# Kernel optimization log

Measured on AMD Instinct MI355X. Metric: run time of the kernel, lower is better.

The kernel has to match this reference:

```python
import jax, jax.numpy as jnp
import numpy as np

NE, NPROC, E, D = 50000, 25000, 200000, 128
L, T = 3, 4  # layers, edge types: 0:e->e, 1:e->p, 2:p->p, 3:p->e


def setup_inputs() -> dict:
    key = jax.random.key(0)
    ks = jax.random.split(key, 17)
    s = 1.0 / np.sqrt(D)
    return {
        'x_elem': jax.random.normal(ks[0], (NE, D), jnp.float32),
        'x_proc': jax.random.normal(ks[1], (NPROC, D), jnp.float32),
        'W_src': jax.random.normal(ks[2], (L, T, D, D), jnp.float32) * s,
        'W_dst': jax.random.normal(ks[3], (L, T, D, D), jnp.float32) * s,
        'att_src': jax.random.normal(ks[4], (L, T, D), jnp.float32) * s,
        'att_dst': jax.random.normal(ks[5], (L, T, D), jnp.float32) * s,
        'bias': jax.random.normal(ks[6], (L, T, D), jnp.float32) * 0.01,
        'lin_W': jax.random.normal(ks[7], (D, 2), jnp.float32) * s,
        'lin_b': jnp.zeros((2,), jnp.float32),
        'ee_src': jax.random.randint(ks[8], (E,), 0, NE),
        'ee_dst': jax.random.randint(ks[9], (E,), 0, NE),
        'ep_src': jax.random.randint(ks[10], (E,), 0, NE),
        'ep_dst': jax.random.randint(ks[11], (E,), 0, NPROC),
        'pp_src': jax.random.randint(ks[12], (E,), 0, NPROC),
        'pp_dst': jax.random.randint(ks[13], (E,), 0, NPROC),
        'pe_src': jax.random.randint(ks[14], (E,), 0, NPROC),
        'pe_dst': jax.random.randint(ks[15], (E,), 0, NE),
    }


def _gat(x_s, x_d, src, dst, n_dst, Ws, Wd, a_s, a_d, b):
    # one GATConv (heads=1, negative_slope=0 -> relu, no self loops)
    hs = x_s @ Ws                       # [Ns, D]
    hd = x_d @ Wd                       # [Nd, D]
    es = hs @ a_s                       # [Ns]
    ed = hd @ a_d                       # [Nd]
    logit = jax.nn.relu(es[src] + ed[dst])              # [E]
    m = jax.ops.segment_max(logit, dst, num_segments=n_dst)
    m = jnp.where(jnp.isfinite(m), m, 0.0)              # empty segments
    w = jnp.exp(logit - m[dst])
    denom = jax.ops.segment_sum(w, dst, num_segments=n_dst)
    alpha = w / jnp.maximum(denom[dst], 1e-16)          # edge softmax per dst
    out = jax.ops.segment_sum(alpha[:, None] * hs[src], dst, num_segments=n_dst)
    return out + b


def reference(x_elem, x_proc, W_src, W_dst, att_src, att_dst, bias, lin_W, lin_b,
              ee_src, ee_dst, ep_src, ep_dst, pp_src, pp_dst, pe_src, pe_dst):
    xe, xp = x_elem, x_proc
    for l in range(L):
        ee = _gat(xe, xe, ee_src, ee_dst, NE, W_src[l, 0], W_dst[l, 0], att_src[l, 0], att_dst[l, 0], bias[l, 0])
        ep = _gat(xe, xp, ep_src, ep_dst, NPROC, W_src[l, 1], W_dst[l, 1], att_src[l, 1], att_dst[l, 1], bias[l, 1])
        pp = _gat(xp, xp, pp_src, pp_dst, NPROC, W_src[l, 2], W_dst[l, 2], att_src[l, 2], att_dst[l, 2], bias[l, 2])
        pe = _gat(xp, xe, pe_src, pe_dst, NE, W_src[l, 3], W_dst[l, 3], att_src[l, 3], att_dst[l, 3], bias[l, 3])
        xe = ee + pe   # to_hetero aggr='sum' per destination node type
        xp = ep + pp
    x = jnp.concatenate([xe, xp], axis=0) @ lin_W + lin_b  # G_aggr
    return x.mean(axis=0)  # [2]
```

## Files before the change

kernel.cpp:

```cpp
#include <hip/hip_runtime.h>

#define NE_N 50000
#define NP_N 25000
#define E_N 200000
#define DIM 128
#define LOG2E 1.4426950408889634f
#define NREP 1024

#define NCHK 32
#define CHK_E (E_N / NCHK)
#define TBL 16384

typedef __attribute__((ext_vector_type(8))) short short8;
typedef __attribute__((ext_vector_type(4))) float f32x4;
typedef __attribute__((ext_vector_type(2))) float f32x2;

static __device__ __forceinline__ ushort f2bf(float f) {
  unsigned x = __float_as_uint(f);
  return (ushort)((x + 0x7fffu + ((x >> 16) & 1u)) >> 16);
}
static __device__ __forceinline__ float bf2f(ushort u) {
  return __uint_as_float(((unsigned)u) << 16);
}

static __device__ __forceinline__ void gload_lds16(const void* g, void* l) {
  __builtin_amdgcn_global_load_lds(
      (const __attribute__((address_space(1))) void*)g,
      (__attribute__((address_space(3))) void*)l, 16, 0, 0);
}

#define HIST_BLKS (4 * NCHK)
#define HS_TOT (HIST_BLKS + 12 + 3)
__global__ __launch_bounds__(512) void hist_setup_k(
    const float* __restrict__ W_src, const float* __restrict__ W_dst,
    const float* __restrict__ att_dst, ushort* __restrict__ WbT,
    float* __restrict__ vec, const int* __restrict__ d0,
    const int* __restrict__ d1, const int* __restrict__ d2,
    const int* __restrict__ d3, unsigned char* __restrict__ h0,
    unsigned char* __restrict__ h1, unsigned char* __restrict__ h2,
    unsigned char* __restrict__ h3, ushort* __restrict__ rk0,
    ushort* __restrict__ rk1, ushort* __restrict__ rk2,
    ushort* __restrict__ rk3) {
  __shared__ int keys[TBL];
  __shared__ int cnts[TBL];
  const int blk = blockIdx.x;
  const int tid = threadIdx.x;
  if (blk < HIST_BLKS) {
    const int ty = blk >> 5, c = blk & (NCHK - 1);
    const int NN = (ty == 0 || ty == 3) ? NE_N : NP_N;
    const int* dst = ty == 0 ? d0 : ty == 1 ? d1 : ty == 2 ? d2 : d3;
    unsigned char* h = ty == 0 ? h0 : ty == 1 ? h1 : ty == 2 ? h2 : h3;
    ushort* rk = ty == 0 ? rk0 : ty == 1 ? rk1 : ty == 2 ? rk2 : rk3;
    for (int i = tid; i < TBL; i += 512) { keys[i] = -1; cnts[i] = 0; }
    __syncthreads();
    const int base = c * CHK_E;
    for (int i = tid; i < CHK_E; i += 512) {
      const int e = base + i;
      const int d = dst[e];
      unsigned hsh = ((unsigned)d * 2654435761u) >> 18;
      hsh &= (TBL - 1);
      int lr;
      while (true) {
        int prev = atomicCAS(&keys[hsh], -1, d);
        if (prev == -1 || prev == d) { lr = atomicAdd(&cnts[hsh], 1); break; }
        hsh = (hsh + 1) & (TBL - 1);
      }
      rk[e] = (ushort)lr;
    }
    __syncthreads();
    for (int i = tid; i < TBL; i += 512) {
      int k = keys[i];
      if (k >= 0) h[(size_t)c * NN + k] = (unsigned char)cnts[i];
    }
  } else if (blk < HIST_BLKS + 12) {
    const int w = blk - HIST_BLKS;
    const float* src = W_src + (size_t)w * DIM * DIM;
    ushort* dstw = WbT + (size_t)w * DIM * DIM;
    for (int i = tid; i < DIM * DIM; i += 512) {
      int k = i >> 7, n = i & 127;
      dstw[n * DIM + k] = f2bf(src[i]);
    }
  } else {
    const int b = blk - HIST_BLKS - 12;
    const int lt = b * 4 + (tid >> 7);
    const int i = tid & 127;
    const float* Wd = W_dst + (size_t)lt * DIM * DIM;
    const float* ad = att_dst + lt * DIM;
    float s = 0.f;
#pragma unroll 8
    for (int j = 0; j < DIM; j++) s += Wd[i * DIM + j] * ad[j];
    vec[lt * DIM + i] = s;
  }
}

__global__ __launch_bounds__(256) void scanA_k(
    unsigned char* __restrict__ h0, unsigned char* __restrict__ h1,
    unsigned char* __restrict__ h2, unsigned char* __restrict__ h3,
    int* __restrict__ c0, int* __restrict__ c1, int* __restrict__ c2,
    int* __restrict__ c3, int* __restrict__ part) {
  int ty = blockIdx.y;
  unsigned char* h = ty == 0 ? h0 : ty == 1 ? h1 : ty == 2 ? h2 : h3;
  int* cnt = ty == 0 ? c0 : ty == 1 ? c1 : ty == 2 ? c2 : c3;
  int n = (ty == 0 || ty == 3) ? NE_N : NP_N;
  int nblk = (n + 1023) >> 10;
  if ((int)blockIdx.x >= nblk) return;
  int base = blockIdx.x * 1024 + threadIdx.x * 4;
  int s = 0;
  if (base < n) {
    int run0 = 0, run1 = 0, run2 = 0, run3 = 0;
#pragma unroll
    for (int c = 0; c < NCHK; c++) {
      unsigned* hp = (unsigned*)(h + (size_t)c * n + base);
      unsigned v = *hp;
      *hp = (unsigned)(run0 & 255) | ((unsigned)(run1 & 255) << 8) |
            ((unsigned)(run2 & 255) << 16) | ((unsigned)(run3 & 255) << 24);
      run0 += (int)(v & 255u);
      run1 += (int)((v >> 8) & 255u);
      run2 += (int)((v >> 16) & 255u);
      run3 += (int)((v >> 24) & 255u);
    }
    cnt[base + 0] = run0; cnt[base + 1] = run1;
    cnt[base + 2] = run2; cnt[base + 3] = run3;
    s = run0 + run1 + run2 + run3;
  }
  int lane = threadIdx.x & 63, wid = threadIdx.x >> 6;
#pragma unroll
  for (int off = 32; off > 0; off >>= 1) s += __shfl_xor(s, off, 64);
  __shared__ int ws4[4];
  if (lane == 0) ws4[wid] = s;
  __syncthreads();
  if (threadIdx.x == 0)
    part[ty * 64 + blockIdx.x] = ws4[0] + ws4[1] + ws4[2] + ws4[3];
}

__global__ __launch_bounds__(256) void scanBC_k(
    const int* __restrict__ c0, const int* __restrict__ c1,
    const int* __restrict__ c2, const int* __restrict__ c3,
    int* __restrict__ r0, int* __restrict__ r1, int* __restrict__ r2,
    int* __restrict__ r3, const int* __restrict__ part) {
  int ty = blockIdx.y;
  int bx = blockIdx.x;
  const int* cnt = ty == 0 ? c0 : ty == 1 ? c1 : ty == 2 ? c2 : c3;
  int* rp = ty == 0 ? r0 : ty == 1 ? r1 : ty == 2 ? r2 : r3;
  int n = (ty == 0 || ty == 3) ? NE_N : NP_N;
  int nblk = (n + 1023) >> 10;
  if (bx >= nblk) return;

  __shared__ int s_excl;
  if (threadIdx.x < 64) {
    int pl = threadIdx.x;
    int v = (pl < nblk) ? part[ty * 64 + pl] : 0;
    int sc = v;
#pragma unroll
    for (int off = 1; off < 64; off <<= 1) {
      int t = __shfl_up(sc, off, 64);
      if (pl >= off) sc += t;
    }
    if (pl == bx) s_excl = sc - v;
  }
  if (bx == 0 && threadIdx.x == 0) rp[n] = E_N;
  __syncthreads();

  int base = bx * 1024 + threadIdx.x * 4;
  int v[4];
#pragma unroll
  for (int j = 0; j < 4; j++) v[j] = (base + j < n) ? cnt[base + j] : 0;
  int s = v[0] + v[1] + v[2] + v[3];
  int lane = threadIdx.x & 63, wid = threadIdx.x >> 6;
  int sc = s;
#pragma unroll
  for (int off = 1; off < 64; off <<= 1) {
    int t = __shfl_up(sc, off, 64);
    if (lane >= off) sc += t;
  }
  __shared__ int ws4[4];
  if (lane == 63) ws4[wid] = sc;
  __syncthreads();
  int wbase = 0;
  for (int w = 0; w < wid; w++) wbase += ws4[w];
  int p = s_excl + wbase + sc - s;
#pragma unroll
  for (int j = 0; j < 4; j++) {
    if (base + j < n) rp[base + j] = p;
    p += v[j];
  }
}

#define EBLK ((NE_N + 127) / 128)
#define PBLK ((NP_N + 127) / 128)
#define GEMM_BLK (EBLK + PBLK)
#define FILL_PER_CHK 13
#define FILL_BLKS (4 * NCHK * FILL_PER_CHK)
#define HG2_TOT (GEMM_BLK + FILL_BLKS)

template <bool FP32>
static __device__ __forceinline__ void x_prefetch(
    const void* xb, int rowA, int quad, float4* xraw, short8* xvv) {
  if (FP32) {
    const float* xf32 = (const float*)xb + (size_t)rowA * DIM + quad * 8;
#pragma unroll
    for (int k0 = 0; k0 < 4; k0++) {
      xraw[2 * k0] = *(const float4*)(xf32 + k0 * 32);
      xraw[2 * k0 + 1] = *(const float4*)(xf32 + k0 * 32 + 4);
    }
  } else {
    const ushort* xb16 = (const ushort*)xb + (size_t)rowA * DIM + quad * 8;
#pragma unroll
    for (int k0 = 0; k0 < 4; k0++)
      xvv[k0] = *(const short8*)(xb16 + k0 * 32);
  }
}

template <bool FP32>
static __device__ __forceinline__ void strip_body(
    int row0, int N, int m, int quad, int lane, const short8* wlds,
    const float* dv0, const float* dv1, const float* a0, const float* a1,
    unsigned char* hs0, unsigned char* hs1, float* es0, float* es1,
    float* edA, float* edB, float4* xraw, short8* xvv) {
  float edp0 = 0.f, edp1 = 0.f;
#pragma unroll
  for (int k0 = 0; k0 < 4; k0++) {
    float xf[8];
    if (FP32) {
      float4 f0 = xraw[2 * k0], f1 = xraw[2 * k0 + 1];
      xf[0] = f0.x; xf[1] = f0.y; xf[2] = f0.z; xf[3] = f0.w;
      xf[4] = f1.x; xf[5] = f1.y; xf[6] = f1.z; xf[7] = f1.w;
      short8 xv;
#pragma unroll
      for (int j = 0; j < 8; j++) xv[j] = (short)f2bf(xf[j]);
      xvv[k0] = xv;
    } else {
#pragma unroll
      for (int j = 0; j < 8; j++) xf[j] = bf2f((ushort)xvv[k0][j]);
    }
    int off = k0 * 32 + quad * 8;
    float4 vA0 = *(const float4*)&dv0[off];
    float4 vA1 = *(const float4*)&dv0[off + 4];
    float4 vB0 = *(const float4*)&dv1[off];
    float4 vB1 = *(const float4*)&dv1[off + 4];
    edp0 += xf[0] * vA0.x + xf[1] * vA0.y + xf[2] * vA0.z + xf[3] * vA0.w +
            xf[4] * vA1.x + xf[5] * vA1.y + xf[6] * vA1.z + xf[7] * vA1.w;
    edp1 += xf[0] * vB0.x + xf[1] * vB0.y + xf[2] * vB0.z + xf[3] * vB0.w +
            xf[4] * vB1.x + xf[5] * vB1.y + xf[6] * vB1.z + xf[7] * vB1.w;
  }

  f32x4 acc0[8], acc1[8];
#pragma unroll
  for (int f = 0; f < 8; f++) {
    acc0[f] = (f32x4){0.f, 0.f, 0.f, 0.f};
    acc1[f] = (f32x4){0.f, 0.f, 0.f, 0.f};
  }
#pragma unroll
  for (int k0 = 0; k0 < 4; k0++) {
    const short8 xv = xvv[k0];
#pragma unroll
    for (int f = 0; f < 8; f++) {
      acc0[f] = __builtin_amdgcn_mfma_f32_16x16x32_bf16(
          wlds[(k0 * 8 + f) * 64 + lane], xv, acc0[f], 0, 0, 0);
      acc1[f] = __builtin_amdgcn_mfma_f32_16x16x32_bf16(
          wlds[2048 + (k0 * 8 + f) * 64 + lane], xv, acc1[f], 0, 0, 0);
    }
  }

  const int row = row0 + m;
  edp0 += __shfl_xor(edp0, 16, 64);
  edp0 += __shfl_xor(edp0, 32, 64);
  edp1 += __shfl_xor(edp1, 16, 64);
  edp1 += __shfl_xor(edp1, 32, 64);
  if (quad == 0 && row < N) {
    edA[row] = edp0 * LOG2E;
    edB[row] = edp1 * LOG2E;
  }

#pragma unroll
  for (int set = 0; set < 2; set++) {
    f32x4* acc = set ? acc1 : acc0;
    const float* as = set ? a1 : a0;
    float* es = set ? es1 : es0;
    unsigned char* hs = set ? hs1 : hs0;

    float esum = 0.f;
#pragma unroll
    for (int f = 0; f < 8; f++) {
      float4 av = *(const float4*)&as[f * 16 + quad * 4];
      esum += acc[f][0] * av.x + acc[f][1] * av.y + acc[f][2] * av.z +
              acc[f][3] * av.w;
    }
    esum += __shfl_xor(esum, 16, 64);
    esum += __shfl_xor(esum, 32, 64);
    if (quad == 0 && row < N) es[row] = esum * LOG2E;

    if (row < N) {
#pragma unroll
      for (int f = 0; f < 8; f++) {
        int w = __builtin_amdgcn_cvt_pk_fp8_f32(acc[f][0], acc[f][1], 0, false);
        w = __builtin_amdgcn_cvt_pk_fp8_f32(acc[f][2], acc[f][3], w, true);
        *(unsigned*)&hs[(size_t)row * DIM + f * 16 + quad * 4] = (unsigned)w;
      }
    }
  }
}

template <bool FP32>
static __device__ __forceinline__ void gemm_body(
    int blk, const void* __restrict__ xev, const void* __restrict__ xpv,
    const ushort* __restrict__ WbT, const float* __restrict__ att,
    const float* __restrict__ vec, int l, unsigned char* __restrict__ hsE0,
    unsigned char* __restrict__ hsE1, unsigned char* __restrict__ hsP3,
    unsigned char* __restrict__ hsP2, float* __restrict__ esE0,
    float* __restrict__ esE1, float* __restrict__ esP3,
    float* __restrict__ esP2, float* __restrict__ edEA,
    float* __restrict__ edEB, float* __restrict__ edPA,
    float* __restrict__ edPB) {
  const void* xb;
  const ushort *W0T, *W1T;
  const float *a0, *a1, *dv0, *dv1;
  unsigned char *hs0, *hs1;
  float *es0, *es1, *edA, *edB;
  int N, rbase;
  if (blk < EBLK) {
    xb = xev; N = NE_N; rbase = blk * 128;
    W0T = WbT + (size_t)(l * 4 + 0) * DIM * DIM;
    W1T = WbT + (size_t)(l * 4 + 1) * DIM * DIM;
    a0 = att + (l * 4 + 0) * DIM; a1 = att + (l * 4 + 1) * DIM;
    dv0 = vec + (l * 4 + 0) * DIM; dv1 = vec + (l * 4 + 3) * DIM;
    hs0 = hsE0; hs1 = hsE1; es0 = esE0; es1 = esE1;
    edA = edEA; edB = edEB;
  } else {
    blk -= EBLK; xb = xpv; N = NP_N; rbase = blk * 128;
    W0T = WbT + (size_t)(l * 4 + 3) * DIM * DIM;
    W1T = WbT + (size_t)(l * 4 + 2) * DIM * DIM;
    a0 = att + (l * 4 + 3) * DIM; a1 = att + (l * 4 + 2) * DIM;
    dv0 = vec + (l * 4 + 1) * DIM; dv1 = vec + (l * 4 + 2) * DIM;
    hs0 = hsP3; hs1 = hsP2; es0 = esP3; es1 = esP2;
    edA = edPA; edB = edPB;
  }

  const int wave = threadIdx.x >> 6;
  const int lane = threadIdx.x & 63;
  const int m = lane & 15, quad = lane >> 4;
  const int row0 = rbase + wave * 16;
  int rowL = row0 + m;
  if (rowL >= N) rowL = N - 1;

  float4 xraw[8]; short8 xvv[4];
  x_prefetch<FP32>(xb, rowL, quad, xraw, xvv);

  __shared__ short8 wlds[4096];
  {
    const int i15 = lane & 15, i4 = lane >> 4;
#pragma unroll
    for (int r = 0; r < 8; r++) {
      const int g = r * 8 + wave;
      const int set = g >> 5, k0 = (g >> 3) & 3, f = g & 7;
      const ushort* WT = set ? W1T : W0T;
      gload_lds16(WT + (size_t)(f * 16 + i15) * DIM + k0 * 32 + i4 * 8,
                  &wlds[g * 64]);
    }
  }
  __syncthreads();
  if (row0 >= N) return;

  strip_body<FP32>(row0, N, m, quad, lane, wlds, dv0, dv1, a0, a1,
                   hs0, hs1, es0, es1, edA, edB, xraw, xvv);
}

__global__ __launch_bounds__(512, 4) void gemm_k(
    const ushort* __restrict__ xe, const ushort* __restrict__ xp,
    const ushort* __restrict__ WbT, const float* __restrict__ att,
    const float* __restrict__ vec, int l, unsigned char* __restrict__ hsE0,
    unsigned char* __restrict__ hsE1, unsigned char* __restrict__ hsP3,
    unsigned char* __restrict__ hsP2, float* __restrict__ esE0,
    float* __restrict__ esE1, float* __restrict__ esP3,
    float* __restrict__ esP2, float* __restrict__ edEA,
    float* __restrict__ edEB, float* __restrict__ edPA,
    float* __restrict__ edPB) {
  gemm_body<false>(blockIdx.x, xe, xp, WbT, att, vec, l, hsE0, hsE1, hsP3,
                   hsP2, esE0, esE1, esP3, esP2, edEA, edEB, edPA, edPB);
}

__global__ __launch_bounds__(512, 4) void fill_gemm0_k(
    const float* __restrict__ xe, const float* __restrict__ xp,
    const ushort* __restrict__ WbT, const float* __restrict__ att,
    const float* __restrict__ vec, unsigned char* __restrict__ hsE0,
    unsigned char* __restrict__ hsE1, unsigned char* __restrict__ hsP3,
    unsigned char* __restrict__ hsP2, float* __restrict__ esE0,
    float* __restrict__ esE1, float* __restrict__ esP3,
    float* __restrict__ esP2, float* __restrict__ edEA,
    float* __restrict__ edEB, float* __restrict__ edPA,
    float* __restrict__ edPB, const int* __restrict__ s0,
    const int* __restrict__ s1, const int* __restrict__ s2,
    const int* __restrict__ s3, const int* __restrict__ d0,
    const int* __restrict__ d1, const int* __restrict__ d2,
    const int* __restrict__ d3, const ushort* __restrict__ rk0,
    const ushort* __restrict__ rk1, const ushort* __restrict__ rk2,
    const ushort* __restrict__ rk3, const int* __restrict__ r0,
    const int* __restrict__ r1, const int* __restrict__ r2,
    const int* __restrict__ r3, const unsigned char* __restrict__ h0,
    const unsigned char* __restrict__ h1, const unsigned char* __restrict__ h2,
    const unsigned char* __restrict__ h3, ushort* __restrict__ o0,
    ushort* __restrict__ o1, ushort* __restrict__ o2,
    ushort* __restrict__ o3) {
  const int blk = blockIdx.x;
  if (blk < GEMM_BLK) {
    gemm_body<true>(blk, xe, xp, WbT, att, vec, 0, hsE0, hsE1, hsP3, hsP2,
                    esE0, esE1, esP3, esP2, edEA, edEB, edPA, edPB);
  } else {
    const int fb = blk - GEMM_BLK;
    const int x = fb & 7, q = fb >> 3;
    const int g = ((q & 15) << 3) | x;
    const int j = q >> 4;
    const int i = j * 512 + threadIdx.x;
    if (i >= CHK_E) return;
    const int ty = g >> 5, c = g & 31;
    const int e = c * CHK_E + i;
    const int NN = (ty == 0 || ty == 3) ? NE_N : NP_N;
    const int* src = ty == 0 ? s0 : ty == 1 ? s1 : ty == 2 ? s2 : s3;
    const int* dst = ty == 0 ? d0 : ty == 1 ? d1 : ty == 2 ? d2 : d3;
    const ushort* rk = ty == 0 ? rk0 : ty == 1 ? rk1 : ty == 2 ? rk2 : rk3;
    const int* rp = ty == 0 ? r0 : ty == 1 ? r1 : ty == 2 ? r2 : r3;
    const unsigned char* ho = ty == 0 ? h0 : ty == 1 ? h1 : ty == 2 ? h2 : h3;
    ushort* out = ty == 0 ? o0 : ty == 1 ? o1 : ty == 2 ? o2 : o3;
    const int dd = dst[e];
    out[rp[dd] + (int)ho[(size_t)c * NN + dd] + (int)rk[e]] =
        (ushort)src[e];
  }
}

__global__ __launch_bounds__(256) void gat_gather_all(
    const int* __restrict__ rp0, const ushort* __restrict__ ss0,
    const int* __restrict__ rp1, const ushort* __restrict__ ss1,
    const int* __restrict__ rp2, const ushort* __restrict__ ss2,
    const int* __restrict__ rp3, const ushort* __restrict__ ss3,
    const float* __restrict__ esE0, const unsigned char* __restrict__ hsE0,
    const float* __restrict__ esE1, const unsigned char* __restrict__ hsE1,
    const float* __restrict__ esP3, const unsigned char* __restrict__ hsP3,
    const float* __restrict__ esP2, const unsigned char* __restrict__ hsP2,
    const float* __restrict__ edEA, const float* __restrict__ edEB,
    const float* __restrict__ edPA, const float* __restrict__ edPB,
    const float* __restrict__ bias, int l, ushort* __restrict__ outxe,
    ushort* __restrict__ outxp, int to_csum, float* __restrict__ csum_rep) {
  const int lane = threadIdx.x & 63;
  const int wv = threadIdx.x >> 6;
  const int half = (lane >> 3) & 1;
  const int sub = lane & 7;
  const int wid = (blockIdx.x * 256 + threadIdx.x) >> 4;
  const bool active = wid < NE_N + NP_N;

  const float *b0 = bias, *b1 = bias;
  ushort* outb = outxe;
  int node = 0;
  int beg = 0, end = 0;
  const ushort* ss = ss0;
  const float* es = esE0;
  const unsigned char* hs = hsE0;
  float edv = 0.f;

  if (active) {
    if (wid < NE_N) {
      node = wid;
      if (half == 0) { ss = ss0; es = esE0; hs = hsE0; edv = edEA[node];
                       beg = rp0[node]; end = rp0[node + 1]; }
      else           { ss = ss3; es = esP3; hs = hsP3; edv = edEB[node];
                       beg = rp3[node]; end = rp3[node + 1]; }
      b0 = bias + (l * 4 + 0) * DIM; b1 = bias + (l * 4 + 3) * DIM;
      outb = outxe;
    } else {
      node = wid - NE_N;
      if (half == 0) { ss = ss1; es = esE1; hs = hsE1; edv = edPA[node];
                       beg = rp1[node]; end = rp1[node + 1]; }
      else           { ss = ss2; es = esP2; hs = hsP2; edv = edPB[node];
                       beg = rp2[node]; end = rp2[node + 1]; }
      b0 = bias + (l * 4 + 1) * DIM; b1 = bias + (l * 4 + 2) * DIM;
      outb = outxp;
    }
  }

  f32x2 acc2[8];
#pragma unroll
  for (int j = 0; j < 8; j++) acc2[j] = (f32x2){0.f, 0.f};
  float sw = 0.f;

  float esC = 0.f;
  uint4 hC = make_uint4(0, 0, 0, 0);
  if (beg < end) {
    const int s0v = ss[beg];
    esC = es[s0v];
    hC = *(const uint4*)&hs[(size_t)s0v * DIM + sub * 16];
  }
  for (int e = beg; e < end; e++) {
    const int en = (e + 1 < end) ? e + 1 : e;
    const int sn = ss[en];
    const float esN = es[sn];
    const uint4 hN = *(const uint4*)&hs[(size_t)sn * DIM + sub * 16];

    const float w = exp2f(fmaxf(esC + edv, 0.f));
    sw += w;
    const f32x2 w2 = {w, w};
    acc2[0] += w2 * __builtin_amdgcn_cvt_pk_f32_fp8((int)hC.x, false);
    acc2[1] += w2 * __builtin_amdgcn_cvt_pk_f32_fp8((int)hC.x, true);
    acc2[2] += w2 * __builtin_amdgcn_cvt_pk_f32_fp8((int)hC.y, false);
    acc2[3] += w2 * __builtin_amdgcn_cvt_pk_f32_fp8((int)hC.y, true);
    acc2[4] += w2 * __builtin_amdgcn_cvt_pk_f32_fp8((int)hC.z, false);
    acc2[5] += w2 * __builtin_amdgcn_cvt_pk_f32_fp8((int)hC.z, true);
    acc2[6] += w2 * __builtin_amdgcn_cvt_pk_f32_fp8((int)hC.w, false);
    acc2[7] += w2 * __builtin_amdgcn_cvt_pk_f32_fp8((int)hC.w, true);
    esC = esN;
    hC = hN;
  }

  const float inv = 1.f / fmaxf(sw, 1e-16f);
#pragma unroll
  for (int j = 0; j < 8; j++) {
    acc2[j].x *= inv;
    acc2[j].y *= inv;
    f32x2 t;
    t.x = __shfl_xor(acc2[j].x, 8, 64);
    t.y = __shfl_xor(acc2[j].y, 8, 64);
    acc2[j] += t;
  }

  if (to_csum) {
#pragma unroll
    for (int j = 0; j < 8; j++) {
      f32x2 t;
      t.x = __shfl_xor(acc2[j].x, 16, 64);
      t.y = __shfl_xor(acc2[j].y, 16, 64);
      acc2[j] += t;
      t.x = __shfl_xor(acc2[j].x, 32, 64);
      t.y = __shfl_xor(acc2[j].y, 32, 64);
      acc2[j] += t;
    }
    __shared__ float lsum[4][DIM];
    if (lane < 8) {
#pragma unroll
      for (int j = 0; j < 8; j++)
        *(float2*)&lsum[wv][sub * 16 + 2 * j] =
            make_float2(acc2[j].x, acc2[j].y);
    }
    __syncthreads();
    if (threadIdx.x < DIM) {
      float s = lsum[0][threadIdx.x] + lsum[1][threadIdx.x] +
                lsum[2][threadIdx.x] + lsum[3][threadIdx.x];
      float* rep = csum_rep + (size_t)(blockIdx.x & (NREP - 1)) * DIM;
      unsafeAtomicAdd(&rep[threadIdx.x], s);
    }
  } else if (active && half == 0) {
    unsigned ow[8];
#pragma unroll
    for (int j = 0; j < 8; j++) {
      const int d = sub * 16 + 2 * j;
      float2 bb0 = *(const float2*)&b0[d];
      float2 bb1 = *(const float2*)&b1[d];
      unsigned lo = f2bf(acc2[j].x + bb0.x + bb1.x);
      unsigned hi = f2bf(acc2[j].y + bb0.y + bb1.y);
      ow[j] = lo | (hi << 16);
    }
    uint4* op = (uint4*)&outb[(size_t)node * DIM + sub * 16];
    op[0] = make_uint4(ow[0], ow[1], ow[2], ow[3]);
    op[1] = make_uint4(ow[4], ow[5], ow[6], ow[7]);
  }
}

__global__ __launch_bounds__(512) void final_proj(
    const float* __restrict__ csum_rep, const float* __restrict__ bias,
    const float* __restrict__ lin_W, const float* __restrict__ lin_b,
    float* __restrict__ out) {
  __shared__ float parts[4][DIM];
  __shared__ float col[DIM];
  const int k = threadIdx.x & 127;
  const int pt = threadIdx.x >> 7;
  float s = 0.f;
#pragma unroll 8
  for (int r = pt * (NREP / 4); r < (pt + 1) * (NREP / 4); r++)
    s += csum_rep[(size_t)r * DIM + k];
  parts[pt][k] = s;
  __syncthreads();
  if (threadIdx.x < DIM) {
    const float* bE0 = bias + (2 * 4 + 0) * DIM;
    const float* bE1 = bias + (2 * 4 + 3) * DIM;
    const float* bP0 = bias + (2 * 4 + 1) * DIM;
    const float* bP1 = bias + (2 * 4 + 2) * DIM;
    col[k] = parts[0][k] + parts[1][k] + parts[2][k] + parts[3][k] +
             (float)NE_N * (bE0[k] + bE1[k]) +
             (float)NP_N * (bP0[k] + bP1[k]);
  }
  __syncthreads();
  if (threadIdx.x < 2) {
    float acc = 0.f;
#pragma unroll 8
    for (int j = 0; j < DIM; j++) acc += col[j] * lin_W[j * 2 + threadIdx.x];
    out[threadIdx.x] = acc / (float)(NE_N + NP_N) + lin_b[threadIdx.x];
  }
}

extern "C" void kernel_launch(void* const* d_in, const int* in_sizes, int n_in,
                              void* d_out, int out_size, void* d_ws,
                              size_t ws_size, hipStream_t stream) {
  const float* x_elem  = (const float*)d_in[0];
  const float* x_proc  = (const float*)d_in[1];
  const float* W_src   = (const float*)d_in[2];
  const float* W_dst   = (const float*)d_in[3];
  const float* att_src = (const float*)d_in[4];
  const float* att_dst = (const float*)d_in[5];
  const float* bias    = (const float*)d_in[6];
  const float* lin_W   = (const float*)d_in[7];
  const float* lin_b   = (const float*)d_in[8];
  const int* esrc[4] = {(const int*)d_in[9],  (const int*)d_in[11],
                        (const int*)d_in[13], (const int*)d_in[15]};
  const int* edst[4] = {(const int*)d_in[10], (const int*)d_in[12],
                        (const int*)d_in[14], (const int*)d_in[16]};

  char* p = (char*)d_ws;
  ushort* xe_bf[2]; ushort* xp_bf[2];
  xe_bf[0] = (ushort*)p; p += (size_t)NE_N * DIM * 2;
  xe_bf[1] = (ushort*)p; p += (size_t)NE_N * DIM * 2;
  xp_bf[0] = (ushort*)p; p += (size_t)NP_N * DIM * 2;
  xp_bf[1] = (ushort*)p; p += (size_t)NP_N * DIM * 2;
  unsigned char* hsE0 = (unsigned char*)p; p += (size_t)NE_N * DIM;
  unsigned char* hsE1 = (unsigned char*)p; p += (size_t)NE_N * DIM;
  unsigned char* hsP3 = (unsigned char*)p; p += (size_t)NP_N * DIM;
  unsigned char* hsP2 = (unsigned char*)p; p += (size_t)NP_N * DIM;
  ushort* WbT = (ushort*)p; p += (size_t)12 * DIM * DIM * 2;
  float* esE0 = (float*)p; p += (size_t)NE_N * 4;
  float* esE1 = (float*)p; p += (size_t)NE_N * 4;
  float* esP3 = (float*)p; p += (size_t)NP_N * 4;
  float* esP2 = (float*)p; p += (size_t)NP_N * 4;
  float* edEA = (float*)p; p += (size_t)NE_N * 4;
  float* edEB = (float*)p; p += (size_t)NE_N * 4;
  float* edPA = (float*)p; p += (size_t)NP_N * 4;
  float* edPB = (float*)p; p += (size_t)NP_N * 4;
  float* vec = (float*)p; p += 12 * DIM * 4;
  int* parti = (int*)p; p += 4 * 64 * 4;
  float* csum_rep = (float*)p; p += (size_t)NREP * DIM * 4;
  unsigned char* hh[4];
  hh[0] = (unsigned char*)p; p += (size_t)NE_N * NCHK;
  hh[1] = (unsigned char*)p; p += (size_t)NP_N * NCHK;
  hh[2] = (unsigned char*)p; p += (size_t)NP_N * NCHK;
  hh[3] = (unsigned char*)p; p += (size_t)NE_N * NCHK;
  int* cnt[4];
  for (int t = 0; t < 4; t++) { cnt[t] = (int*)p; p += (NE_N + 4) * 4; }
  int* rp[4];
  for (int t = 0; t < 4; t++) { rp[t] = (int*)p; p += (NE_N + 4) * 4; }
  ushort* ssrc[4];
  for (int t = 0; t < 4; t++) { ssrc[t] = (ushort*)p; p += (size_t)E_N * 2; }
  ushort* rank[4];
  for (int t = 0; t < 4; t++) { rank[t] = (ushort*)p; p += (size_t)E_N * 2; }

  hipMemsetAsync(csum_rep, 0,
                 (size_t)NREP * DIM * 4 +
                     (size_t)(2 * NE_N + 2 * NP_N) * NCHK,
                 stream);

  hist_setup_k<<<HS_TOT, 512, 0, stream>>>(
      W_src, W_dst, att_dst, WbT, vec, edst[0], edst[1], edst[2], edst[3],
      hh[0], hh[1], hh[2], hh[3], rank[0], rank[1], rank[2], rank[3]);

  scanA_k<<<dim3(49, 4), 256, 0, stream>>>(hh[0], hh[1], hh[2], hh[3],
                                           cnt[0], cnt[1], cnt[2], cnt[3],
                                           parti);
  scanBC_k<<<dim3(49, 4), 256, 0, stream>>>(cnt[0], cnt[1], cnt[2], cnt[3],
                                            rp[0], rp[1], rp[2], rp[3], parti);

  fill_gemm0_k<<<HG2_TOT, 512, 0, stream>>>(
      x_elem, x_proc, WbT, att_src, vec, hsE0, hsE1, hsP3, hsP2, esE0, esE1,
      esP3, esP2, edEA, edEB, edPA, edPB, esrc[0], esrc[1], esrc[2], esrc[3],
      edst[0], edst[1], edst[2], edst[3], rank[0], rank[1], rank[2], rank[3],
      rp[0], rp[1], rp[2], rp[3], hh[0], hh[1], hh[2], hh[3],
      ssrc[0], ssrc[1], ssrc[2], ssrc[3]);

  int c = 0;
  for (int l = 0; l < 3; l++) {
    if (l > 0) {
      gemm_k<<<GEMM_BLK, 512, 0, stream>>>(
          xe_bf[c], xp_bf[c], WbT, att_src, vec, l, hsE0, hsE1, hsP3, hsP2,
          esE0, esE1, esP3, esP2, edEA, edEB, edPA, edPB);
    }
    int to_csum = (l == 2) ? 1 : 0;
    gat_gather_all<<<(NE_N + NP_N + 15) / 16, 256, 0, stream>>>(
        rp[0], ssrc[0], rp[1], ssrc[1], rp[2], ssrc[2], rp[3], ssrc[3], esE0,
        hsE0, esE1, hsE1, esP3, hsP3, esP2, hsP2, edEA, edEB, edPA, edPB,
        bias, l, xe_bf[1 - c], xp_bf[1 - c], to_csum, csum_rep);
    c = 1 - c;
  }

  final_proj<<<1, 512, 0, stream>>>(csum_rep, bias, lin_W, lin_b,
                                    (float*)d_out);
}
```

Measured before the change: 354.3 us.

## Sort destination nodes by in-degree to balance gather workload per wavefront

Adds a three-kernel counting sort (block histograms, offset scan, scatter) that orders element and processor nodes by combined in-degree, capped at 64 bins. The gather kernel then looks up its node through this permutation, so the 16-lane groups sharing a wavefront handle nodes with similar edge counts and less time is lost to divergence. In exchange it adds three small kernel launches per call plus an indirection load, and output writes are no longer in node order, which weakens write coalescing and locality.

```diff
diff --git a/kernel.cpp b/kernel.cpp
--- a/kernel.cpp
+++ b/kernel.cpp
@@ -10,6 +10,10 @@
 #define NCHK 32
 #define CHK_E (E_N / NCHK)
 #define TBL 16384
+
+#define NBIN 64
+#define EB49 ((NE_N + 1023) / 1024)
+#define PB25 ((NP_N + 1023) / 1024)
 
 typedef __attribute__((ext_vector_type(8))) short short8;
 typedef __attribute__((ext_vector_type(4))) float f32x4;
@@ -183,6 +187,94 @@
   for (int j = 0; j < 4; j++) {
     if (base + j < n) rp[base + j] = p;
     p += v[j];
+  }
+}
+
+__global__ __launch_bounds__(256) void sortA_k(
+    const int* __restrict__ rp0, const int* __restrict__ rp3,
+    const int* __restrict__ rp1, const int* __restrict__ rp2,
+    unsigned* __restrict__ bh) {
+  const int ty = blockIdx.y;
+  const int n = ty ? NP_N : NE_N;
+  const int nblk = ty ? PB25 : EB49;
+  if ((int)blockIdx.x >= nblk) return;
+  const int* rpA = ty ? rp1 : rp0;
+  const int* rpB = ty ? rp2 : rp3;
+  __shared__ unsigned h[NBIN];
+  if (threadIdx.x < NBIN) h[threadIdx.x] = 0;
+  __syncthreads();
+  const int base = blockIdx.x * 1024 + threadIdx.x * 4;
+#pragma unroll
+  for (int j = 0; j < 4; j++) {
+    const int node = base + j;
+    if (node < n) {
+      int key = (rpA[node + 1] - rpA[node]) + (rpB[node + 1] - rpB[node]);
+      if (key > NBIN - 1) key = NBIN - 1;
+      atomicAdd(&h[key], 1u);
+    }
+  }
+  __syncthreads();
+  if (threadIdx.x < NBIN)
+    bh[((size_t)ty * NBIN + threadIdx.x) * EB49 + blockIdx.x] = h[threadIdx.x];
+}
+
+__global__ __launch_bounds__(256) void sortB_k(const unsigned* __restrict__ bh,
+                                               unsigned* __restrict__ off) {
+  __shared__ unsigned tot[NBIN];
+  __shared__ unsigned binoff[NBIN];
+  const int tid = threadIdx.x;
+  for (int ty = 0; ty < 2; ty++) {
+    const int nblk = ty ? PB25 : EB49;
+    if (tid < NBIN) {
+      unsigned s = 0;
+      for (int b = 0; b < nblk; b++)
+        s += bh[((size_t)ty * NBIN + tid) * EB49 + b];
+      tot[tid] = s;
+    }
+    __syncthreads();
+    if (tid == 0) {
+      unsigned r = 0;
+      for (int k = 0; k < NBIN; k++) { binoff[k] = r; r += tot[k]; }
+    }
+    __syncthreads();
+    if (tid < NBIN) {
+      unsigned r = binoff[tid];
+      for (int b = 0; b < nblk; b++) {
+        off[((size_t)ty * NBIN + tid) * EB49 + b] = r;
+        r += bh[((size_t)ty * NBIN + tid) * EB49 + b];
+      }
+    }
+    __syncthreads();
+  }
+}
+
+__global__ __launch_bounds__(256) void sortC_k(
+    const int* __restrict__ rp0, const int* __restrict__ rp3,
+    const int* __restrict__ rp1, const int* __restrict__ rp2,
+    const unsigned* __restrict__ off, int* __restrict__ permE,
+    int* __restrict__ permP) {
+  const int ty = blockIdx.y;
+  const int n = ty ? NP_N : NE_N;
+  const int nblk = ty ? PB25 : EB49;
+  if ((int)blockIdx.x >= nblk) return;
+  const int* rpA = ty ? rp1 : rp0;
+  const int* rpB = ty ? rp2 : rp3;
+  int* perm = ty ? permP : permE;
+  __shared__ unsigned cur[NBIN];
+  if (threadIdx.x < NBIN)
+    cur[threadIdx.x] =
+        off[((size_t)ty * NBIN + threadIdx.x) * EB49 + blockIdx.x];
+  __syncthreads();
+  const int base = blockIdx.x * 1024 + threadIdx.x * 4;
+#pragma unroll
+  for (int j = 0; j < 4; j++) {
+    const int node = base + j;
+    if (node < n) {
+      int key = (rpA[node + 1] - rpA[node]) + (rpB[node + 1] - rpB[node]);
+      if (key > NBIN - 1) key = NBIN - 1;
+      const unsigned pos = atomicAdd(&cur[key], 1u);
+      perm[pos] = node;
+    }
   }
 }
 
@@ -439,7 +531,8 @@
     const float* __restrict__ edEA, const float* __restrict__ edEB,
     const float* __restrict__ edPA, const float* __restrict__ edPB,
     const float* __restrict__ bias, int l, ushort* __restrict__ outxe,
-    ushort* __restrict__ outxp, int to_csum, float* __restrict__ csum_rep) {
+    ushort* __restrict__ outxp, int to_csum, float* __restrict__ csum_rep,
+    const int* __restrict__ permE, const int* __restrict__ permP) {
   const int lane = threadIdx.x & 63;
   const int wv = threadIdx.x >> 6;
   const int half = (lane >> 3) & 1;
@@ -458,7 +551,7 @@
 
   if (active) {
     if (wid < NE_N) {
-      node = wid;
+      node = permE[wid];
       if (half == 0) { ss = ss0; es = esE0; hs = hsE0; edv = edEA[node];
                        beg = rp0[node]; end = rp0[node + 1]; }
       else           { ss = ss3; es = esP3; hs = hsP3; edv = edEB[node];
@@ -466,7 +559,7 @@
       b0 = bias + (l * 4 + 0) * DIM; b1 = bias + (l * 4 + 3) * DIM;
       outb = outxe;
     } else {
-      node = wid - NE_N;
+      node = permP[wid - NE_N];
       if (half == 0) { ss = ss1; es = esE1; hs = hsE1; edv = edPA[node];
                        beg = rp1[node]; end = rp1[node + 1]; }
       else           { ss = ss2; es = esP2; hs = hsP2; edv = edPB[node];
@@ -646,6 +739,10 @@
   for (int t = 0; t < 4; t++) { ssrc[t] = (ushort*)p; p += (size_t)E_N * 2; }
   ushort* rank[4];
   for (int t = 0; t < 4; t++) { rank[t] = (ushort*)p; p += (size_t)E_N * 2; }
+  int* permE = (int*)p; p += (size_t)NE_N * 4;
+  int* permP = (int*)p; p += (size_t)NP_N * 4;
+  unsigned* bh = (unsigned*)p; p += (size_t)2 * NBIN * EB49 * 4;
+  unsigned* boff = (unsigned*)p; p += (size_t)2 * NBIN * EB49 * 4;
 
   hipMemsetAsync(csum_rep, 0,
                  (size_t)NREP * DIM * 4 +
@@ -661,6 +758,11 @@
                                            parti);
   scanBC_k<<<dim3(49, 4), 256, 0, stream>>>(cnt[0], cnt[1], cnt[2], cnt[3],
                                             rp[0], rp[1], rp[2], rp[3], parti);
+
+  sortA_k<<<dim3(EB49, 2), 256, 0, stream>>>(rp[0], rp[3], rp[1], rp[2], bh);
+  sortB_k<<<1, 256, 0, stream>>>(bh, boff);
+  sortC_k<<<dim3(EB49, 2), 256, 0, stream>>>(rp[0], rp[3], rp[1], rp[2],
+                                             boff, permE, permP);
 
   fill_gemm0_k<<<HG2_TOT, 512, 0, stream>>>(
       x_elem, x_proc, WbT, att_src, vec, hsE0, hsE1, hsP3, hsP2, esE0, esE1,
@@ -680,7 +782,7 @@
     gat_gather_all<<<(NE_N + NP_N + 15) / 16, 256, 0, stream>>>(
         rp[0], ssrc[0], rp[1], ssrc[1], rp[2], ssrc[2], rp[3], ssrc[3], esE0,
         hsE0, esE1, hsE1, esP3, hsP3, esP2, hsP2, edEA, edEB, edPA, edPB,
-        bias, l, xe_bf[1 - c], xp_bf[1 - c], to_csum, csum_rep);
+        bias, l, xe_bf[1 - c], xp_bf[1 - c], to_csum, csum_rep, permE, permP);
     c = 1 - c;
   }
 
```

Measured after the change: 375.2 us. +5.9%, slower.
